# Kernel optimization log

Measured on AMD Instinct MI355X. Metric: run time of the kernel, lower is better.

Reference implementation:

```python
import jax, jax.numpy as jnp
import numpy as np

L, N, E, NODE_D, EDGE_D, H = 3, 50000, 800000, 64, 16, 128
EPS = 1e-5


def _ln(x, g, b):
    mu = jnp.mean(x, axis=-1, keepdims=True)
    var = jnp.var(x, axis=-1, keepdims=True)
    return (x - mu) * jax.lax.rsqrt(var + EPS) * g + b


def setup_inputs() -> dict:
    key = jax.random.key(0)
    ks = jax.random.split(key, 16)
    inp = {
        "x": jax.random.normal(ks[0], (N, NODE_D), dtype=jnp.float32),
        "edge_index": jax.random.randint(ks[1], (2, E), 0, N, dtype=jnp.int64 if jax.config.jax_enable_x64 else jnp.int32),
        "edge_attr": jax.random.normal(ks[2], (E, EDGE_D), dtype=jnp.float32),
        # node_embed: Linear(node_dim, H) + LayerNorm
        "node_W": jax.random.normal(ks[3], (H, NODE_D), dtype=jnp.float32) * (2.0 / H) ** 0.5,
        "node_b": jnp.zeros((H,), jnp.float32),
        "node_ln_g": jnp.ones((H,), jnp.float32),
        "node_ln_b": jnp.zeros((H,), jnp.float32),
        # per-layer GINConv params, stacked on leading layer dim
        "edge_W": jax.random.normal(ks[4], (L, H, EDGE_D), dtype=jnp.float32) * (2.0 / H) ** 0.5,
        "edge_b": jnp.zeros((L, H), jnp.float32),
        "edge_ln_g": jnp.ones((L, H), jnp.float32),
        "edge_ln_b": jnp.zeros((L, H), jnp.float32),
        "sl_attr": jax.random.normal(ks[5], (L, 1, EDGE_D), dtype=jnp.float32),
        "mlp_W1": jax.random.normal(ks[6], (L, 2 * H, H), dtype=jnp.float32) * (1.0 / H) ** 0.5,
        "mlp_b1": jnp.zeros((L, 2 * H), jnp.float32),
        "mlp_W2": jax.random.normal(ks[7], (L, H, 2 * H), dtype=jnp.float32) * (1.0 / (2 * H)) ** 0.5,
        "mlp_b2": jnp.zeros((L, H), jnp.float32),
        # BatchNorm1d affine params (batch-stat / training-mode math)
        "bn_g": jnp.ones((L, H), jnp.float32),
        "bn_b": jnp.zeros((L, H), jnp.float32),
    }
    return inp


def reference(x, edge_index, edge_attr, node_W, node_b, node_ln_g, node_ln_b,
              edge_W, edge_b, edge_ln_g, edge_ln_b, sl_attr,
              mlp_W1, mlp_b1, mlp_W2, mlp_b2, bn_g, bn_b):
    n = x.shape[0]
    # augmented edge list with self loops appended (add_self_loops)
    loop = jnp.arange(n, dtype=edge_index.dtype)
    src = jnp.concatenate([edge_index[0], loop])  # [E+N]
    dst = jnp.concatenate([edge_index[1], loop])  # [E+N]

    # node_embed: Linear -> LN -> ReLU
    h = jax.nn.relu(_ln(x @ node_W.T + node_b, node_ln_g, node_ln_b))

    for l in range(L):
        # edge_embed on [original edges ; learned self-loop attr]
        sl = jnp.broadcast_to(sl_attr[l], (n, EDGE_D))
        ea = jnp.concatenate([edge_attr, sl], axis=0)          # [E+N, edge_dim]
        ea = jax.nn.relu(_ln(ea @ edge_W[l].T + edge_b[l], edge_ln_g[l], edge_ln_b[l]))
        # message: gather x_j + edge_attr; aggregate: scatter-add to dst
        msg = h[src] + ea                                      # [E+N, H]
        aggr = jax.ops.segment_sum(msg, dst, num_segments=n)   # [N, H]
        # update MLP: Linear -> GELU -> Linear (dropout inactive at eval)
        z = jax.nn.gelu(aggr @ mlp_W1[l].T + mlp_b1[l], approximate=False)
        hl = z @ mlp_W2[l].T + mlp_b2[l]
        # BatchNorm1d (training-mode batch statistics over node dim)
        mu = jnp.mean(hl, axis=0, keepdims=True)
        var = jnp.var(hl, axis=0, keepdims=True)
        hl = (hl - mu) * jax.lax.rsqrt(var + EPS) * bn_g[l] + bn_b[l]
        if l != L - 1:
            hl = jax.nn.relu(hl)  # drop_ratio = 0 -> dropout is identity
        h = hl
    return h
```

## Files before the change

### kernel.cpp

```cpp
#include <hip/hip_runtime.h>
#include <cstdint>
#include <cstddef>

#define HD 128
#define EDGED 16
#define NODED 64
#define LN_EPS 1e-5f

typedef __bf16 bf16x8 __attribute__((ext_vector_type(8)));
typedef float  f32x4  __attribute__((ext_vector_type(4)));

__device__ __forceinline__ float gelu_exact(float x) {
    return 0.5f * x * (1.0f + erff(x * 0.7071067811865475f));
}

__global__ void wconv_k(const float* __restrict__ in, __bf16* __restrict__ hi,
                        __bf16* __restrict__ lo, int n) {
    int i = blockIdx.x * blockDim.x + threadIdx.x;
    if (i < n) {
        float v = in[i];
        __bf16 h = (__bf16)v;
        hi[i] = h;
        lo[i] = (__bf16)(v - (float)h);
    }
}


__global__ void hist_k(const int* __restrict__ ei, int* __restrict__ cnt, int E) {
    int e = blockIdx.x * blockDim.x + threadIdx.x;
    if (e < E) atomicAdd(&cnt[ei[E + e]], 1);
}

__global__ void scan1_k(const int* __restrict__ in, int* __restrict__ out,
                        int* __restrict__ bsum, int n) {
    __shared__ int lds[256];
    int t = threadIdx.x;
    int i = blockIdx.x * 256 + t;
    int v = (i < n) ? in[i] : 0;
    lds[t] = v;
    __syncthreads();
#pragma unroll
    for (int o = 1; o < 256; o <<= 1) {
        int u = (t >= o) ? lds[t - o] : 0;
        __syncthreads();
        lds[t] += u;
        __syncthreads();
    }
    if (i < n) out[i] = lds[t] - v;
    if (t == 255) bsum[blockIdx.x] = lds[255];
}

__global__ void scan2_k(const int* __restrict__ bsum, int* __restrict__ boff, int nb) {
    __shared__ int lds[256];
    int t = threadIdx.x;
    int v = (t < nb) ? bsum[t] : 0;
    lds[t] = v;
    __syncthreads();
#pragma unroll
    for (int o = 1; o < 256; o <<= 1) {
        int u = (t >= o) ? lds[t - o] : 0;
        __syncthreads();
        lds[t] += u;
        __syncthreads();
    }
    if (t < nb) boff[t] = lds[t] - v;
}

__global__ void scan3_k(int* __restrict__ rs, int* __restrict__ cursor,
                        const int* __restrict__ boff, int n, int E) {
    int i = blockIdx.x * 256 + threadIdx.x;
    if (i < n) {
        int v = rs[i] + boff[blockIdx.x];
        rs[i] = v;
        cursor[i] = v;
    }
    if (i == 0) rs[n] = E;
}

__global__ void scatter_k(const int* __restrict__ ei, int* __restrict__ cursor,
                          int2* __restrict__ es, int E) {
    int e = blockIdx.x * blockDim.x + threadIdx.x;
    if (e < E) {
        int dst = ei[E + e];
        int slot = atomicAdd(&cursor[dst], 1);
        es[slot] = make_int2(ei[e], e);
    }
}

__global__ void prep_k(const float* __restrict__ edge_W, const float* __restrict__ edge_b,
                       const float* __restrict__ edge_g, const float* __restrict__ edge_be,
                       const float* __restrict__ sl_attr, float* __restrict__ Wg3,
                       float* __restrict__ bg3, float* __restrict__ M3,
                       float* __restrict__ v3, float* __restrict__ s03,
                       float* __restrict__ slv3)
{
    const int l = blockIdx.x;
    const float* W = edge_W + (size_t)l * HD * EDGED;
    const float* b = edge_b + l * HD;
    const float* g = edge_g + l * HD;
    __shared__ float Wp[HD * EDGED];
    __shared__ float bp[HD];
    __shared__ float wm[EDGED];
    __shared__ float Msh[256];
    __shared__ float vsh[EDGED];
    __shared__ float ash[EDGED];
    __shared__ float bmS, s0sh;
    const int t = threadIdx.x;
#pragma unroll
    for (int m = 0; m < 8; ++m) Wp[m * 256 + t] = W[m * 256 + t];
    __syncthreads();
    if (t < EDGED) {
        float s = 0.f;
        for (int c = 0; c < HD; ++c) s += Wp[c * EDGED + t];
        wm[t] = s * (1.f / HD);
    } else if (t == EDGED) {
        float s = 0.f;
        for (int c = 0; c < HD; ++c) s += b[c];
        bmS = s * (1.f / HD);
    }
    __syncthreads();
    if (t < HD) bp[t] = b[t] - bmS;
    __syncthreads();
#pragma unroll
    for (int m = 0; m < 8; ++m) {
        int idx = m * 256 + t;
        int c = idx >> 4, k = idx & 15;
        float val = Wp[idx] - wm[k];
        Wp[idx] = val;
        Wg3[(size_t)l * 2048 + k * HD + c] = val * g[c];
    }
    if (t < HD) bg3[l * HD + t] = bp[t] * g[t];
    __syncthreads();
    {
        int k = t >> 4, j = t & 15;
        float s = 0.f;
        for (int c = 0; c < HD; ++c) s += Wp[c * EDGED + k] * Wp[c * EDGED + j];
        Msh[t] = s;
        M3[l * 256 + t] = s;
    }
    if (t < EDGED) {
        float s = 0.f;
        for (int c = 0; c < HD; ++c) s += Wp[c * EDGED + t] * bp[c];
        vsh[t] = 2.f * s;
        v3[l * EDGED + t] = 2.f * s;
        ash[t] = sl_attr[l * EDGED + t];
    } else if (t == EDGED) {
        float s = 0.f;
        for (int c = 0; c < HD; ++c) s += bp[c] * bp[c];
        s0sh = s;
        s03[l] = s;
    }
    __syncthreads();
    if (t < HD) {
        float q = s0sh;
#pragma unroll
        for (int k = 0; k < EDGED; ++k) {
            float tk = vsh[k];
#pragma unroll
            for (int j = 0; j < EDGED; ++j) tk = fmaf(Msh[k * 16 + j], ash[j], tk);
            q = fmaf(ash[k], tk, q);
        }
        float inv = rsqrtf(q * (1.f / HD) + LN_EPS);
        float y = 0.f;
#pragma unroll
        for (int k = 0; k < EDGED; ++k) y = fmaf(Wp[t * EDGED + k], ash[k], y);
        slv3[l * HD + t] = fmaxf(fmaf(fmaf(y, g[t], bg3[l * HD + t]), inv, edge_be[l * HD + t]), 0.f);
    }
}

__launch_bounds__(256)
__global__ void einv_k(const int2* __restrict__ es, const float* __restrict__ eattr,
                       const float* __restrict__ M3, const float* __restrict__ v3,
                       const float* __restrict__ s03, float* __restrict__ einv, int E)
{
    __shared__ float Ms[3 * 256];
    __shared__ float vs[3 * 16];
    __shared__ float s0s[4];
    const int t = threadIdx.x;
    for (int i = t; i < 768; i += 256) Ms[i] = M3[i];
    if (t < 48) vs[t] = v3[t];
    if (t < 3) s0s[t] = s03[t];
    __syncthreads();
    int slot = blockIdx.x * 256 + t;
    if (slot >= E) return;
    int eid = es[slot].y;
    const float4* ap = (const float4*)(eattr + (size_t)eid * EDGED);
    float4 A0 = ap[0], A1 = ap[1], A2 = ap[2], A3 = ap[3];
    float a[16] = {A0.x, A0.y, A0.z, A0.w, A1.x, A1.y, A1.z, A1.w,
                   A2.x, A2.y, A2.z, A2.w, A3.x, A3.y, A3.z, A3.w};
#pragma unroll
    for (int l = 0; l < 3; ++l) {
        float q = s0s[l];
#pragma unroll
        for (int k = 0; k < 16; ++k) {
            const float* Mr = &Ms[l * 256 + k * 16];
            float tk = vs[l * 16 + k];
#pragma unroll
            for (int j = 0; j < 16; ++j) tk = fmaf(Mr[j], a[j], tk);
            q = fmaf(a[k], tk, q);
        }
        einv[(size_t)l * E + slot] = rsqrtf(q * (1.f / HD) + LN_EPS);
    }
}

template<int K, int NC, int ACT, int STATS, int OUTBF>
__launch_bounds__(256)
__global__ void mgemm_k(const __bf16* __restrict__ Ahi, const __bf16* __restrict__ Alo,
                        const __bf16* __restrict__ Whi, const __bf16* __restrict__ Wlo,
                        const float* __restrict__ bias, float* __restrict__ C,
                        __bf16* __restrict__ Chi, __bf16* __restrict__ Clo,
                        int M, float* __restrict__ stats)
{
    constexpr int RG = 2;
    constexpr int NT = 4;
    constexpr int NK = K / 32;
    __shared__ float st_lds[2][64];

    const int t    = threadIdx.x;
    const int lane = t & 63;
    const int wv   = t >> 6;
    const int ln15 = lane & 15;
    const int quad = lane >> 4;
    const int row_base = blockIdx.x * 128 + wv * 32;
    const int col0 = blockIdx.y * 64;

    f32x4 acc[RG][NT];
#pragma unroll
    for (int g = 0; g < RG; ++g)
#pragma unroll
        for (int nt = 0; nt < NT; ++nt)
#pragma unroll
            for (int r = 0; r < 4; ++r) acc[g][nt][r] = 0.f;

    size_t arow[RG];
#pragma unroll
    for (int g = 0; g < RG; ++g) {
        int row = row_base + g * 16 + ln15;
        row = row < M ? row : M - 1;
        arow[g] = (size_t)row * K + quad * 8;
    }
    size_t brow[NT];
#pragma unroll
    for (int nt = 0; nt < NT; ++nt)
        brow[nt] = (size_t)(col0 + nt * 16 + ln15) * K + quad * 8;

    bf16x8 a0h[RG], a0l[RG], a1h[RG], a1l[RG];
    bf16x8 b0h[NT], b0l[NT], b1h[NT], b1l[NT];

#define LD_A(kc, AH, AL) { \
    _Pragma("unroll") \
    for (int g = 0; g < RG; ++g) { \
        AH[g] = *(const bf16x8*)(Ahi + arow[g] + (kc)); \
        AL[g] = *(const bf16x8*)(Alo + arow[g] + (kc)); \
    } }
#define LD_B(kc, BH, BL) { \
    _Pragma("unroll") \
    for (int nt = 0; nt < NT; ++nt) { \
        BH[nt] = *(const bf16x8*)(Whi + brow[nt] + (kc)); \
        BL[nt] = *(const bf16x8*)(Wlo + brow[nt] + (kc)); \
    } }
#define DO_MFMA(AH, AL, BH, BL) { \
    _Pragma("unroll") \
    for (int nt = 0; nt < NT; ++nt) { \
        _Pragma("unroll") \
        for (int g = 0; g < RG; ++g) { \
            acc[g][nt] = __builtin_amdgcn_mfma_f32_16x16x32_bf16(AH[g], BH[nt], acc[g][nt], 0, 0, 0); \
            acc[g][nt] = __builtin_amdgcn_mfma_f32_16x16x32_bf16(AH[g], BL[nt], acc[g][nt], 0, 0, 0); \
            acc[g][nt] = __builtin_amdgcn_mfma_f32_16x16x32_bf16(AL[g], BH[nt], acc[g][nt], 0, 0, 0); \
        } } }

    LD_A(0, a0h, a0l);
    LD_B(0, b0h, b0l);
    for (int s = 0; s < NK; s += 2) {
        LD_A((s + 1) * 32, a1h, a1l);
        LD_B((s + 1) * 32, b1h, b1l);
        DO_MFMA(a0h, a0l, b0h, b0l);
        if (s + 2 < NK) {
            LD_A((s + 2) * 32, a0h, a0l);
            LD_B((s + 2) * 32, b0h, b0l);
        }
        DO_MFMA(a1h, a1l, b1h, b1l);
    }
#undef LD_A
#undef LD_B
#undef DO_MFMA

    if (STATS) {
        if (t < 64) { st_lds[0][t] = 0.f; st_lds[1][t] = 0.f; }
        __syncthreads();
    }

    float bv[NT];
#pragma unroll
    for (int nt = 0; nt < NT; ++nt) bv[nt] = bias[col0 + nt * 16 + ln15];

    float s1[NT], s2[NT];
#pragma unroll
    for (int nt = 0; nt < NT; ++nt) { s1[nt] = 0.f; s2[nt] = 0.f; }

#pragma unroll
    for (int g = 0; g < RG; ++g)
#pragma unroll
        for (int r = 0; r < 4; ++r) {
            int row = row_base + g * 16 + quad * 4 + r;
            if (row < M) {
#pragma unroll
                for (int nt = 0; nt < NT; ++nt) {
                    float v = acc[g][nt][r] + bv[nt];
                    if (ACT == 1) v = gelu_exact(v);
                    size_t ci = (size_t)row * NC + col0 + nt * 16 + ln15;
                    if (OUTBF) {
                        __bf16 hh = (__bf16)v;
                        Chi[ci] = hh;
                        Clo[ci] = (__bf16)(v - (float)hh);
                    } else {
                        C[ci] = v;
                    }
                    if (STATS) { s1[nt] += v; s2[nt] += v * v; }
                }
            }
        }

    if (STATS) {
#pragma unroll
        for (int nt = 0; nt < NT; ++nt) {
            atomicAdd(&st_lds[0][nt * 16 + ln15], s1[nt]);
            atomicAdd(&st_lds[1][nt * 16 + ln15], s2[nt]);
        }
        __syncthreads();
        if (t < 64) {
            atomicAdd(&stats[col0 + t],      st_lds[0][t]);
            atomicAdd(&stats[HD + col0 + t], st_lds[1][t]);
        }
    }
}

__global__ void ln_relu_k(const float* __restrict__ y, const float* __restrict__ gam,
                          const float* __restrict__ bet, float* __restrict__ h, int N)
{
    int lane = threadIdx.x & 63;
    int c0 = lane * 2;
    float2 g2 = *(const float2*)&gam[c0];
    float2 b2 = *(const float2*)&bet[c0];
    int wid = (blockIdx.x * blockDim.x + threadIdx.x) >> 6;
    int nw  = (gridDim.x * blockDim.x) >> 6;
    for (int n = wid; n < N; n += nw) {
        float2 v = *(const float2*)&y[(size_t)n * HD + c0];
        float s = v.x + v.y;
        float q = v.x * v.x + v.y * v.y;
#pragma unroll
        for (int o = 32; o > 0; o >>= 1) { s += __shfl_xor(s, o, 64); q += __shfl_xor(q, o, 64); }
        float mu  = s * (1.f / 128.f);
        float inv = rsqrtf(q * (1.f / 128.f) - mu * mu + LN_EPS);
        float2 r;
        r.x = fmaxf(fmaf((v.x - mu) * inv, g2.x, b2.x), 0.f);
        r.y = fmaxf(fmaf((v.y - mu) * inv, g2.y, b2.y), 0.f);
        *(float2*)&h[(size_t)n * HD + c0] = r;
    }
}

__launch_bounds__(256)
__global__ void pull3_k(const float* __restrict__ h, const int2* __restrict__ es,
                        const int* __restrict__ rs, const float* __restrict__ eattr,
                        const float* __restrict__ einv, const float* __restrict__ slv,
                        const float* __restrict__ Wg, const float* __restrict__ bg,
                        const float* __restrict__ bet, __bf16* __restrict__ Ahi,
                        __bf16* __restrict__ Alo, int N)
{
    __shared__ float alds_all[4][64 * EDGED];
    const int t = threadIdx.x;
    const int lane = t & 63;
    const int wv = t >> 6;
    float* alds = alds_all[wv];

    const int c1 = lane, c2 = lane + 64;
    float w1[16], w2[16];
#pragma unroll
    for (int k = 0; k < 16; ++k) {
        w1[k] = Wg[k * HD + c1];
        w2[k] = Wg[k * HD + c2];
    }
    const float bg1 = bg[c1], bg2 = bg[c2];
    const float bt1 = bet[c1], bt2 = bet[c2];

    const int n = (blockIdx.x << 2) + wv;
    if (n >= N) return;

    float acc1 = h[(size_t)n * HD + c1] + slv[c1];
    float acc2 = h[(size_t)n * HD + c2] + slv[c2];

    const int beg = rs[n], end = rs[n + 1];
    for (int s0 = beg; s0 < end; s0 += 64) {
        int m = end - s0; if (m > 64) m = 64;
        int2 se = make_int2(0, 0);
        float iv = 0.f;
        if (lane < m) { se = es[s0 + lane]; iv = einv[s0 + lane]; }
#pragma unroll
        for (int it = 0; it < 4; ++it) {
            int idx  = (it << 6) + lane;
            int jsrc = idx >> 2;
            int eid  = __shfl(se.y, jsrc, 64);
            if (idx < (m << 2)) {
                float4 av = *(const float4*)&eattr[(size_t)eid * EDGED + ((idx & 3) << 2)];
                *(float4*)&alds[idx << 2] = av;
            }
        }
        asm volatile("s_waitcnt lgkmcnt(0)" ::: "memory");
        for (int j = 0; j < m; ++j) {
            float4 A0 = *(const float4*)&alds[j * EDGED];
            float4 A1 = *(const float4*)&alds[j * EDGED + 4];
            float4 A2 = *(const float4*)&alds[j * EDGED + 8];
            float4 A3 = *(const float4*)&alds[j * EDGED + 12];
            int   src = __shfl(se.x, j, 64);
            float ivj = __shfl(iv,   j, 64);
            float hv1 = h[(size_t)src * HD + c1];
            float hv2 = h[(size_t)src * HD + c2];
            float a[16] = {A0.x, A0.y, A0.z, A0.w, A1.x, A1.y, A1.z, A1.w,
                           A2.x, A2.y, A2.z, A2.w, A3.x, A3.y, A3.z, A3.w};
            float p1 = bg1, q1 = 0.f, p2 = bg2, q2 = 0.f;
#pragma unroll
            for (int k = 0; k < 16; k += 2) {
                p1 = fmaf(a[k],     w1[k],     p1);
                q1 = fmaf(a[k + 1], w1[k + 1], q1);
                p2 = fmaf(a[k],     w2[k],     p2);
                q2 = fmaf(a[k + 1], w2[k + 1], q2);
            }
            float v1 = fmaxf(fmaf(p1 + q1, ivj, bt1), 0.f);
            float v2 = fmaxf(fmaf(p2 + q2, ivj, bt2), 0.f);
            acc1 += v1 + hv1;
            acc2 += v2 + hv2;
        }
    }
    __bf16 h1 = (__bf16)acc1, h2 = (__bf16)acc2;
    Ahi[(size_t)n * HD + c1] = h1;
    Alo[(size_t)n * HD + c1] = (__bf16)(acc1 - (float)h1);
    Ahi[(size_t)n * HD + c2] = h2;
    Alo[(size_t)n * HD + c2] = (__bf16)(acc2 - (float)h2);
}

__global__ void bn_k(const float* __restrict__ hl, const float* __restrict__ stats,
                     const float* __restrict__ gam, const float* __restrict__ bet,
                     float* __restrict__ out, int total4, float invN, int relu)
{
    int idx = blockIdx.x * blockDim.x + threadIdx.x;
    if (idx < total4) {
        int c4 = idx & 31;
        float4 x  = ((const float4*)hl)[idx];
        float4 s1 = ((const float4*)stats)[c4];
        float4 s2 = ((const float4*)stats)[32 + c4];
        float4 g  = ((const float4*)gam)[c4];
        float4 b  = ((const float4*)bet)[c4];
        float4 r;
        {
            float m = s1.x * invN; float v = s2.x * invN - m * m;
            r.x = fmaf((x.x - m) * rsqrtf(v + LN_EPS), g.x, b.x);
        }
        {
            float m = s1.y * invN; float v = s2.y * invN - m * m;
            r.y = fmaf((x.y - m) * rsqrtf(v + LN_EPS), g.y, b.y);
        }
        {
            float m = s1.z * invN; float v = s2.z * invN - m * m;
            r.z = fmaf((x.z - m) * rsqrtf(v + LN_EPS), g.z, b.z);
        }
        {
            float m = s1.w * invN; float v = s2.w * invN - m * m;
            r.w = fmaf((x.w - m) * rsqrtf(v + LN_EPS), g.w, b.w);
        }
        if (relu) {
            r.x = fmaxf(r.x, 0.f); r.y = fmaxf(r.y, 0.f);
            r.z = fmaxf(r.z, 0.f); r.w = fmaxf(r.w, 0.f);
        }
        ((float4*)out)[idx] = r;
    }
}

extern "C" void kernel_launch(void* const* d_in, const int* in_sizes, int n_in,
                              void* d_out, int out_size, void* d_ws, size_t ws_size,
                              hipStream_t stream)
{
    const float* x       = (const float*)d_in[0];
    const int*   ei      = (const int*)d_in[1];
    const float* eattr   = (const float*)d_in[2];
    const float* node_W  = (const float*)d_in[3];
    const float* node_b  = (const float*)d_in[4];
    const float* node_g  = (const float*)d_in[5];
    const float* node_be = (const float*)d_in[6];
    const float* edge_W  = (const float*)d_in[7];
    const float* edge_b  = (const float*)d_in[8];
    const float* edge_g  = (const float*)d_in[9];
    const float* edge_be = (const float*)d_in[10];
    const float* sl_attr = (const float*)d_in[11];
    const float* W1      = (const float*)d_in[12];
    const float* b1      = (const float*)d_in[13];
    const float* W2      = (const float*)d_in[14];
    const float* b2      = (const float*)d_in[15];
    const float* bn_g    = (const float*)d_in[16];
    const float* bn_b    = (const float*)d_in[17];

    const int N = in_sizes[0] / NODED;
    const int E = in_sizes[1] / 2;

    char* base = (char*)d_ws;
    size_t off = 0;
    auto take = [&](size_t nbytes) -> void* {
        void* p = base + off;
        off = (off + nbytes + 15) & ~(size_t)15;
        return p;
    };
    float*  h      = (float*)take((size_t)N * HD * 4);
    float*  z      = (float*)take((size_t)N * HD * 4);
    __bf16* aghi   = (__bf16*)take((size_t)N * HD * 2);
    __bf16* aglo   = (__bf16*)take((size_t)N * HD * 2);
    __bf16* zhi    = (__bf16*)take((size_t)N * 256 * 2);
    __bf16* zlo    = (__bf16*)take((size_t)N * 256 * 2);
    __bf16* xhi    = (__bf16*)take((size_t)N * NODED * 2);
    __bf16* xlo    = (__bf16*)take((size_t)N * NODED * 2);
    float*  slv3   = (float*)take(3 * HD * 4);
    float*  stats  = (float*)take(3 * 256 * 4);
    int*    cnt    = (int*)take((size_t)N * 4);
    int*    cursor = (int*)take((size_t)N * 4);
    int*    bsum   = (int*)take(256 * 4);
    int*    boff   = (int*)take(256 * 4);
    int*    rs     = (int*)take(((size_t)N + 2) * 4);
    int2*   es     = (int2*)take((size_t)E * 8);
    float*  einv   = (float*)take((size_t)3 * E * 4);
    float*  Wg3    = (float*)take(3 * 2048 * 4);
    float*  bg3    = (float*)take(3 * HD * 4);
    float*  M3     = (float*)take(3 * 256 * 4);
    float*  v3     = (float*)take(3 * 16 * 4);
    float*  s03    = (float*)take(4 * 4);
    __bf16* nWhi   = (__bf16*)take((size_t)HD * NODED * 2);
    __bf16* nWlo   = (__bf16*)take((size_t)HD * NODED * 2);
    __bf16* W1hi   = (__bf16*)take((size_t)3 * 256 * HD * 2);
    __bf16* W1lo   = (__bf16*)take((size_t)3 * 256 * HD * 2);
    __bf16* W2hi   = (__bf16*)take((size_t)3 * HD * 256 * 2);
    __bf16* W2lo   = (__bf16*)take((size_t)3 * HD * 256 * 2);

    wconv_k<<<(HD * NODED + 255) / 256, 256, 0, stream>>>(node_W, nWhi, nWlo, HD * NODED);
    wconv_k<<<(3 * 256 * HD + 255) / 256, 256, 0, stream>>>(W1, W1hi, W1lo, 3 * 256 * HD);
    wconv_k<<<(3 * 256 * HD + 255) / 256, 256, 0, stream>>>(W2, W2hi, W2lo, 3 * 256 * HD);
    wconv_k<<<((int)((size_t)N * NODED + 255) / 256), 256, 0, stream>>>(x, xhi, xlo, N * NODED);

    prep_k<<<3, 256, 0, stream>>>(edge_W, edge_b, edge_g, edge_be, sl_attr,
                                  Wg3, bg3, M3, v3, s03, slv3);

    const int eblocks = (E + 255) / 256;
    const int nblocks = (N + 255) / 256;
    hipMemsetAsync(cnt, 0, (size_t)N * sizeof(int), stream);
    hist_k<<<eblocks, 256, 0, stream>>>(ei, cnt, E);
    scan1_k<<<nblocks, 256, 0, stream>>>(cnt, rs, bsum, N);
    scan2_k<<<1, 256, 0, stream>>>(bsum, boff, nblocks);
    scan3_k<<<nblocks, 256, 0, stream>>>(rs, cursor, boff, N, E);
    scatter_k<<<eblocks, 256, 0, stream>>>(ei, cursor, es, E);

    einv_k<<<eblocks, 256, 0, stream>>>(es, eattr, M3, v3, s03, einv, E);

    const int total4  = N * (HD / 4);
    const int vblocks = (total4 + 255) / 256;
    const int pblocks = (N + 3) / 4;
    const int gb128   = (N + 127) / 128;

    mgemm_k<NODED, HD, 0, 0, 0><<<dim3(gb128, 2), 256, 0, stream>>>(
        xhi, xlo, nWhi, nWlo, node_b, z, nullptr, nullptr, N, nullptr);
    ln_relu_k<<<pblocks, 256, 0, stream>>>(z, node_g, node_be, h, N);

    hipMemsetAsync(stats, 0, 3 * 256 * sizeof(float), stream);

    for (int l = 0; l < 3; ++l) {
        pull3_k<<<pblocks, 256, 0, stream>>>(h, es, rs, eattr, einv + (size_t)l * E,
                                             slv3 + l * HD, Wg3 + (size_t)l * 2048,
                                             bg3 + l * HD, edge_be + l * HD,
                                             aghi, aglo, N);

        mgemm_k<HD, 256, 1, 0, 1><<<dim3(gb128, 4), 256, 0, stream>>>(
            aghi, aglo, W1hi + (size_t)l * 256 * HD, W1lo + (size_t)l * 256 * HD,
            b1 + l * 256, nullptr, zhi, zlo, N, nullptr);

        mgemm_k<256, HD, 0, 1, 0><<<dim3(gb128, 2), 256, 0, stream>>>(
            zhi, zlo, W2hi + (size_t)l * HD * 256, W2lo + (size_t)l * HD * 256,
            b2 + l * HD, (float*)d_out, nullptr, nullptr, N, stats + l * 256);

        bn_k<<<vblocks, 256, 0, stream>>>((const float*)d_out, stats + l * 256,
                                          bn_g + l * HD, bn_b + l * HD,
                                          (l < 2) ? h : (float*)d_out, total4, 1.f / N, (l < 2) ? 1 : 0);
    }
}
```

Measured before the change: 1.007 ms.

## Permute edge attributes into CSR order once and vectorize pull kernel gathers

The einv kernel now also writes edge attributes and source indices into CSR-sorted order, so the per-layer pull kernel reads contiguous attribute rows instead of gathering by edge id. The pull kernel switches to float2 per lane (two adjacent channels), unrolls the edge loop by four to issue several h-row gathers at once, and packs its bf16 outputs into 32-bit stores. This trades one extra write of E×16 floats plus source indices against three layers of random attribute gathers and fewer, wider memory operations.

```diff
diff --git a/kernel.cpp b/kernel.cpp
--- a/kernel.cpp
+++ b/kernel.cpp
@@ -171,7 +171,8 @@
 __launch_bounds__(256)
 __global__ void einv_k(const int2* __restrict__ es, const float* __restrict__ eattr,
                        const float* __restrict__ M3, const float* __restrict__ v3,
-                       const float* __restrict__ s03, float* __restrict__ einv, int E)
+                       const float* __restrict__ s03, float* __restrict__ einv,
+                       float* __restrict__ attr_p, int* __restrict__ srcp, int E)
 {
     __shared__ float Ms[3 * 256];
     __shared__ float vs[3 * 16];
@@ -183,9 +184,12 @@
     __syncthreads();
     int slot = blockIdx.x * 256 + t;
     if (slot >= E) return;
-    int eid = es[slot].y;
-    const float4* ap = (const float4*)(eattr + (size_t)eid * EDGED);
+    int2 se = es[slot];
+    srcp[slot] = se.x;
+    const float4* ap = (const float4*)(eattr + (size_t)se.y * EDGED);
     float4 A0 = ap[0], A1 = ap[1], A2 = ap[2], A3 = ap[3];
+    float4* op = (float4*)(attr_p + (size_t)slot * EDGED);
+    op[0] = A0; op[1] = A1; op[2] = A2; op[3] = A3;
     float a[16] = {A0.x, A0.y, A0.z, A0.w, A1.x, A1.y, A1.z, A1.w,
                    A2.x, A2.y, A2.z, A2.w, A3.x, A3.y, A3.z, A3.w};
 #pragma unroll
@@ -360,8 +364,8 @@
 }
 
 __launch_bounds__(256)
-__global__ void pull3_k(const float* __restrict__ h, const int2* __restrict__ es,
-                        const int* __restrict__ rs, const float* __restrict__ eattr,
+__global__ void pull4_k(const float* __restrict__ h, const int* __restrict__ srcp,
+                        const int* __restrict__ rs, const float* __restrict__ attr_p,
                         const float* __restrict__ einv, const float* __restrict__ slv,
                         const float* __restrict__ Wg, const float* __restrict__ bg,
                         const float* __restrict__ bet, __bf16* __restrict__ Ahi,
@@ -373,69 +377,91 @@
     const int wv = t >> 6;
     float* alds = alds_all[wv];
 
-    const int c1 = lane, c2 = lane + 64;
-    float w1[16], w2[16];
+    const int c0 = lane * 2;
+    float w0[16], w1[16];
 #pragma unroll
     for (int k = 0; k < 16; ++k) {
-        w1[k] = Wg[k * HD + c1];
-        w2[k] = Wg[k * HD + c2];
-    }
-    const float bg1 = bg[c1], bg2 = bg[c2];
-    const float bt1 = bet[c1], bt2 = bet[c2];
+        float2 wp = *(const float2*)&Wg[k * HD + c0];
+        w0[k] = wp.x; w1[k] = wp.y;
+    }
+    const float2 bgv = *(const float2*)&bg[c0];
+    const float2 btv = *(const float2*)&bet[c0];
 
     const int n = (blockIdx.x << 2) + wv;
     if (n >= N) return;
 
-    float acc1 = h[(size_t)n * HD + c1] + slv[c1];
-    float acc2 = h[(size_t)n * HD + c2] + slv[c2];
+    const float2 hself = *(const float2*)&h[(size_t)n * HD + c0];
+    const float2 slvv  = *(const float2*)&slv[c0];
+    float acc0 = hself.x + slvv.x;
+    float acc1 = hself.y + slvv.y;
 
     const int beg = rs[n], end = rs[n + 1];
     for (int s0 = beg; s0 < end; s0 += 64) {
         int m = end - s0; if (m > 64) m = 64;
-        int2 se = make_int2(0, 0);
-        float iv = 0.f;
-        if (lane < m) { se = es[s0 + lane]; iv = einv[s0 + lane]; }
+        int   srcv = 0;
+        float ivv  = 0.f;
+        if (lane < m) { srcv = srcp[s0 + lane]; ivv = einv[s0 + lane]; }
+        const float4* src4 = (const float4*)(attr_p + (size_t)s0 * EDGED);
 #pragma unroll
         for (int it = 0; it < 4; ++it) {
-            int idx  = (it << 6) + lane;
-            int jsrc = idx >> 2;
-            int eid  = __shfl(se.y, jsrc, 64);
-            if (idx < (m << 2)) {
-                float4 av = *(const float4*)&eattr[(size_t)eid * EDGED + ((idx & 3) << 2)];
-                *(float4*)&alds[idx << 2] = av;
-            }
+            int idx = (it << 6) + lane;
+            if (idx < (m << 2)) *(float4*)&alds[idx << 2] = src4[idx];
         }
         asm volatile("s_waitcnt lgkmcnt(0)" ::: "memory");
-        for (int j = 0; j < m; ++j) {
-            float4 A0 = *(const float4*)&alds[j * EDGED];
-            float4 A1 = *(const float4*)&alds[j * EDGED + 4];
-            float4 A2 = *(const float4*)&alds[j * EDGED + 8];
-            float4 A3 = *(const float4*)&alds[j * EDGED + 12];
-            int   src = __shfl(se.x, j, 64);
-            float ivj = __shfl(iv,   j, 64);
-            float hv1 = h[(size_t)src * HD + c1];
-            float hv2 = h[(size_t)src * HD + c2];
-            float a[16] = {A0.x, A0.y, A0.z, A0.w, A1.x, A1.y, A1.z, A1.w,
-                           A2.x, A2.y, A2.z, A2.w, A3.x, A3.y, A3.z, A3.w};
-            float p1 = bg1, q1 = 0.f, p2 = bg2, q2 = 0.f;
-#pragma unroll
-            for (int k = 0; k < 16; k += 2) {
-                p1 = fmaf(a[k],     w1[k],     p1);
-                q1 = fmaf(a[k + 1], w1[k + 1], q1);
-                p2 = fmaf(a[k],     w2[k],     p2);
-                q2 = fmaf(a[k + 1], w2[k + 1], q2);
-            }
-            float v1 = fmaxf(fmaf(p1 + q1, ivj, bt1), 0.f);
-            float v2 = fmaxf(fmaf(p2 + q2, ivj, bt2), 0.f);
-            acc1 += v1 + hv1;
-            acc2 += v2 + hv2;
-        }
-    }
-    __bf16 h1 = (__bf16)acc1, h2 = (__bf16)acc2;
-    Ahi[(size_t)n * HD + c1] = h1;
-    Alo[(size_t)n * HD + c1] = (__bf16)(acc1 - (float)h1);
-    Ahi[(size_t)n * HD + c2] = h2;
-    Alo[(size_t)n * HD + c2] = (__bf16)(acc2 - (float)h2);
+
+#define EDGE_BODY(JJ, IVJ, HVJ) { \
+            const float* ar = &alds[(JJ) * EDGED]; \
+            float4 A0 = *(const float4*)ar,       A1 = *(const float4*)(ar + 4); \
+            float4 A2 = *(const float4*)(ar + 8), A3 = *(const float4*)(ar + 12); \
+            float a[16] = {A0.x, A0.y, A0.z, A0.w, A1.x, A1.y, A1.z, A1.w, \
+                           A2.x, A2.y, A2.z, A2.w, A3.x, A3.y, A3.z, A3.w}; \
+            float p0 = bgv.x, q0 = 0.f, p1 = bgv.y, q1 = 0.f; \
+            _Pragma("unroll") \
+            for (int k = 0; k < 16; k += 2) { \
+                p0 = fmaf(a[k],     w0[k],     p0); \
+                q0 = fmaf(a[k + 1], w0[k + 1], q0); \
+                p1 = fmaf(a[k],     w1[k],     p1); \
+                q1 = fmaf(a[k + 1], w1[k + 1], q1); \
+            } \
+            acc0 += fmaxf(fmaf(p0 + q0, IVJ, btv.x), 0.f) + HVJ.x; \
+            acc1 += fmaxf(fmaf(p1 + q1, IVJ, btv.y), 0.f) + HVJ.y; \
+        }
+
+        int j = 0;
+        for (; j + 4 <= m; j += 4) {
+            int s_0 = __shfl(srcv, j,     64);
+            int s_1 = __shfl(srcv, j + 1, 64);
+            int s_2 = __shfl(srcv, j + 2, 64);
+            int s_3 = __shfl(srcv, j + 3, 64);
+            float i0 = __shfl(ivv, j,     64);
+            float i1 = __shfl(ivv, j + 1, 64);
+            float i2 = __shfl(ivv, j + 2, 64);
+            float i3 = __shfl(ivv, j + 3, 64);
+            float2 h0 = *(const float2*)&h[(size_t)s_0 * HD + c0];
+            float2 h1 = *(const float2*)&h[(size_t)s_1 * HD + c0];
+            float2 h2 = *(const float2*)&h[(size_t)s_2 * HD + c0];
+            float2 h3 = *(const float2*)&h[(size_t)s_3 * HD + c0];
+            EDGE_BODY(j,     i0, h0);
+            EDGE_BODY(j + 1, i1, h1);
+            EDGE_BODY(j + 2, i2, h2);
+            EDGE_BODY(j + 3, i3, h3);
+        }
+        for (; j < m; ++j) {
+            int s_  = __shfl(srcv, j, 64);
+            float ij = __shfl(ivv, j, 64);
+            float2 hj = *(const float2*)&h[(size_t)s_ * HD + c0];
+            EDGE_BODY(j, ij, hj);
+        }
+#undef EDGE_BODY
+    }
+    __bf16 b0 = (__bf16)acc0, b1 = (__bf16)acc1;
+    union { __bf16 b[2]; unsigned u; } ph, pl;
+    ph.b[0] = b0;
+    ph.b[1] = b1;
+    pl.b[0] = (__bf16)(acc0 - (float)b0);
+    pl.b[1] = (__bf16)(acc1 - (float)b1);
+    *(unsigned*)&Ahi[(size_t)n * HD + c0] = ph.u;
+    *(unsigned*)&Alo[(size_t)n * HD + c0] = pl.u;
 }
 
 __global__ void bn_k(const float* __restrict__ hl, const float* __restrict__ stats,
@@ -525,6 +551,8 @@
     int*    rs     = (int*)take(((size_t)N + 2) * 4);
     int2*   es     = (int2*)take((size_t)E * 8);
     float*  einv   = (float*)take((size_t)3 * E * 4);
+    float*  attr_p = (float*)take((size_t)E * EDGED * 4);
+    int*    srcp   = (int*)take((size_t)E * 4);
     float*  Wg3    = (float*)take(3 * 2048 * 4);
     float*  bg3    = (float*)take(3 * HD * 4);
     float*  M3     = (float*)take(3 * 256 * 4);
@@ -554,7 +582,7 @@
     scan3_k<<<nblocks, 256, 0, stream>>>(rs, cursor, boff, N, E);
     scatter_k<<<eblocks, 256, 0, stream>>>(ei, cursor, es, E);
 
-    einv_k<<<eblocks, 256, 0, stream>>>(es, eattr, M3, v3, s03, einv, E);
+    einv_k<<<eblocks, 256, 0, stream>>>(es, eattr, M3, v3, s03, einv, attr_p, srcp, E);
 
     const int total4  = N * (HD / 4);
     const int vblocks = (total4 + 255) / 256;
@@ -568,7 +596,8 @@
     hipMemsetAsync(stats, 0, 3 * 256 * sizeof(float), stream);
 
     for (int l = 0; l < 3; ++l) {
-        pull3_k<<<pblocks, 256, 0, stream>>>(h, es, rs, eattr, einv + (size_t)l * E,
+        pull4_k<<<pblocks, 256, 0, stream>>>(h, srcp, rs, attr_p,
+                                             einv + (size_t)l * E,
                                              slv3 + l * HD, Wg3 + (size_t)l * 2048,
                                              bg3 + l * HD, edge_be + l * HD,
                                              aghi, aglo, N);
```

Result: no change. 999.0 us (-0.8%).
